# Performance work log

Hardware: AMD Instinct MI355X
Metric: run time of the kernel (lower is better)

The kernel has to match this reference:

```python
import jax, jax.numpy as jnp
import numpy as np
from jax import lax

K = 3
PAD = 1
STRIDE = 1


def setup_inputs() -> dict:
    key = jax.random.key(0)
    k1, k2, k3 = jax.random.split(key, 3)
    B, Cin, Cout, H, W = 4, 64, 64, 128, 128
    x = jax.random.normal(k1, (B, Cin, H, W), dtype=jnp.float32)
    # offset-generating conv weight: [2*K*K, Cin, K, K]
    w_offset = jax.random.normal(k2, (2 * K * K, Cin, K, K), dtype=jnp.float32) * 0.05
    # deformable conv weight: [Cout, Cin, K, K]
    w_deform = jax.random.normal(k3, (Cout, Cin, K, K), dtype=jnp.float32) * 0.05
    return {"x": x, "w_offset": w_offset, "w_deform": w_deform}


def _bilinear_sample_one(img, ys, xs):
    # img: [C, H, W]; ys, xs: [K2, Ho, Wo] float sampling coords
    H, W = img.shape[1], img.shape[2]
    y0 = jnp.floor(ys)
    x0 = jnp.floor(xs)
    wy = ys - y0  # frac weights, [K2, Ho, Wo]
    wx = xs - x0

    def gather(yi, xi):
        valid = (yi >= 0) & (yi <= H - 1) & (xi >= 0) & (xi <= W - 1)
        yc = jnp.clip(yi, 0, H - 1).astype(jnp.int32)
        xc = jnp.clip(xi, 0, W - 1).astype(jnp.int32)
        # img[:, yc, xc] -> [C, K2, Ho, Wo]; zero outside (torchvision zero-pad)
        return img[:, yc, xc] * valid[None].astype(img.dtype)

    v00 = gather(y0, x0)
    v01 = gather(y0, x0 + 1)
    v10 = gather(y0 + 1, x0)
    v11 = gather(y0 + 1, x0 + 1)
    w00 = ((1 - wy) * (1 - wx))[None]
    w01 = ((1 - wy) * wx)[None]
    w10 = (wy * (1 - wx))[None]
    w11 = (wy * wx)[None]
    return v00 * w00 + v01 * w01 + v10 * w10 + v11 * w11  # [C, K2, Ho, Wo]


def reference(x, w_offset, w_deform):
    B, Cin, H, W = x.shape
    Cout = w_deform.shape[0]
    K2 = K * K
    # 1) plain conv to produce offsets: [B, 2*K2, H, W]
    offset = lax.conv_general_dilated(
        x, w_offset, window_strides=(STRIDE, STRIDE),
        padding=((PAD, PAD), (PAD, PAD)),
        dimension_numbers=("NCHW", "OIHW", "NCHW"))
    Ho, Wo = offset.shape[2], offset.shape[3]
    # torchvision ordering: channel 2*k = dy, 2*k+1 = dx, taps row-major
    off = offset.reshape(B, K2, 2, Ho, Wo)
    dy, dx = off[:, :, 0], off[:, :, 1]  # [B, K2, Ho, Wo]
    # 2) base sampling grid per kernel tap
    kk = jnp.arange(K2)
    ki = (kk // K).astype(jnp.float32)  # tap row
    kj = (kk % K).astype(jnp.float32)   # tap col
    base_y = (jnp.arange(Ho, dtype=jnp.float32) * STRIDE - PAD)[None, :] + ki[:, None]  # [K2, Ho]
    base_x = (jnp.arange(Wo, dtype=jnp.float32) * STRIDE - PAD)[None, :] + kj[:, None]  # [K2, Wo]
    ys = base_y[None, :, :, None] + dy  # [B, K2, Ho, Wo]
    xs = base_x[None, :, None, :] + dx
    # 3) deformable bilinear gather: [B, Cin, K2, Ho, Wo]
    sampled = jax.vmap(_bilinear_sample_one)(x, ys, xs)
    # 4) weighted accumulation (the conv contraction)
    out = jnp.einsum("ock,bckhw->bohw", w_deform.reshape(Cout, Cin, K2), sampled)
    return out
```

## Files before the change

kernel.cpp:

```cpp
#include <hip/hip_runtime.h>


#define BATCH 4
#define CIN   64
#define COUT  64
#define HH    128
#define WW    128
#define HWPIX (HH*WW)

typedef __attribute__((ext_vector_type(8))) short short8;
typedef __attribute__((ext_vector_type(4))) float floatx4;

__device__ __forceinline__ unsigned short f2bf(float f) {
  unsigned int u = __float_as_uint(f);
  unsigned int r = u + 0x7fffu + ((u >> 16) & 1u);
  return (unsigned short)(r >> 16);
}
__device__ __forceinline__ float bf2f(unsigned short h) { return __uint_as_float(((unsigned int)h) << 16); }
__device__ __forceinline__ float lo16f(unsigned int u) { return __uint_as_float(u << 16); }
__device__ __forceinline__ float hi16f(unsigned int u) { return __uint_as_float(u & 0xffff0000u); }

__device__ __forceinline__ unsigned int bilin2(unsigned int u00, unsigned int u01,
                                               unsigned int u10, unsigned int u11,
                                               float w00, float w01, float w10, float w11) {
  float lo = w00 * lo16f(u00) + w01 * lo16f(u01) + w10 * lo16f(u10) + w11 * lo16f(u11);
  float hi = w00 * hi16f(u00) + w01 * hi16f(u01) + w10 * hi16f(u10) + w11 * hi16f(u11);
  return (unsigned int)f2bf(lo) | ((unsigned int)f2bf(hi) << 16);
}

__device__ __forceinline__ int swz(int a) { return a ^ (((a >> 9) & 3) << 4); }

__global__ __launch_bounds__(256) void pre_kernel(const float* __restrict__ x,
                                                  const float* __restrict__ wo,
                                                  const float* __restrict__ wd,
                                                  unsigned short* __restrict__ xThi,
                                                  unsigned short* __restrict__ xTlo,
                                                  unsigned short* __restrict__ wdA,
                                                  unsigned short* __restrict__ woAhi,
                                                  unsigned short* __restrict__ woAlo) {
  int tid = threadIdx.x;
  if (blockIdx.x < 4096) {
    __shared__ float tile[32][33];
    int t = blockIdx.x;
    int b = t >> 10, rem = t & 1023;
    int c0 = (rem >> 9) * 32, p0 = (rem & 511) * 32;
    int tx = tid & 31, ty = tid >> 5;
    const float* xb = x + (size_t)b * CIN * HWPIX;
    size_t boff = (size_t)b * HWPIX * CIN;
#pragma unroll
    for (int i = 0; i < 4; i++)
      tile[ty + i * 8][tx] = xb[(size_t)(c0 + ty + i * 8) * HWPIX + p0 + tx];
    __syncthreads();
#pragma unroll
    for (int i = 0; i < 2; i++) {
      int tt = tid + i * 256;
      int row = tt >> 4;
      int cp = tt & 15;
      float v0 = tile[cp * 2][row], v1 = tile[cp * 2 + 1][row];
      unsigned short h0 = f2bf(v0), h1 = f2bf(v1);
      unsigned short l0 = f2bf(v0 - bf2f(h0)), l1 = f2bf(v1 - bf2f(h1));
      size_t o = boff + (size_t)(p0 + row) * CIN + c0 + cp * 2;
      *(ushort2*)&xThi[o] = make_ushort2(h0, h1);
      *(ushort2*)&xTlo[o] = make_ushort2(l0, l1);
    }
  } else {
    int t = (blockIdx.x - 4096) * 256 + tid;
    if (t < 36864) {
      int j = t & 7, lane = (t >> 3) & 63, ct = (t >> 9) & 3, kc = (t >> 11) & 1, kk = t >> 12;
      int cout = ct * 16 + (lane & 15);
      int cin  = kc * 32 + (lane >> 4) * 8 + j;
      wdA[t] = f2bf(wd[(size_t)(cout * CIN + cin) * 9 + kk]);
    }
    int t2 = t - 36864;
    if (t2 >= 0 && t2 < 18432) {
      int j = t2 & 7, lane = (t2 >> 3) & 63, ct = (t2 >> 9) & 1, kc = (t2 >> 10) & 1, kk = t2 >> 11;
      int cout = ct * 16 + (lane & 15);
      int cin  = kc * 32 + (lane >> 4) * 8 + j;
      float v = (cout < 18) ? wo[(size_t)(cout * CIN + cin) * 9 + kk] : 0.f;
      unsigned short h = f2bf(v);
      woAhi[t2] = h;
      woAlo[t2] = f2bf(v - bf2f(h));
    }
  }
}

__global__ __launch_bounds__(256) void fused_dcn_kernel(const unsigned short* __restrict__ xThi,
                                                        const unsigned short* __restrict__ xTlo,
                                                        const unsigned short* __restrict__ woAhi,
                                                        const unsigned short* __restrict__ woAlo,
                                                        const unsigned short* __restrict__ wdA,
                                                        float* __restrict__ out) {
  __shared__ unsigned short sBhi[4096];
  __shared__ unsigned short sBlo[4096];
  __shared__ float offL[18 * 64];

  int tid = threadIdx.x;
  int hw = blockIdx.x;
  int bid = (hw & 7) * 128 + (hw >> 3);
  int b = bid >> 8, r = bid & 255, y = r >> 1, x0 = (r & 1) << 6;

  int p1 = tid >> 2, si = tid & 3;
  int lane = tid & 63, w = tid >> 6;

  const unsigned short* xhib = xThi + (size_t)b * HWPIX * CIN;
  const unsigned short* xlob = xTlo + (size_t)b * HWPIX * CIN;

  int wq = p1 >> 4, iq = p1 & 15;
  int kcd = si >> 1, qb = si & 1;
  int wb0 = ((((wq * 2 + kcd) * 64) + qb * 32 + iq) * 8) * 2;
  int wb1 = wb0 + 256;
  unsigned short* stHi0 = (unsigned short*)((char*)sBhi + swz(wb0));
  unsigned short* stHi1 = (unsigned short*)((char*)sBhi + swz(wb1));
  unsigned short* stLo0 = (unsigned short*)((char*)sBlo + swz(wb0));
  unsigned short* stLo1 = (unsigned short*)((char*)sBlo + swz(wb1));
  int rb0 = (w * 2 + 0) * 1024 + lane * 16;
  int rb1 = (w * 2 + 1) * 1024 + lane * 16;
  const short8* rdHi0 = (const short8*)((const char*)sBhi + swz(rb0));
  const short8* rdHi1 = (const short8*)((const char*)sBhi + swz(rb1));
  const short8* rdLo0 = (const short8*)((const char*)sBlo + swz(rb0));
  const short8* rdLo1 = (const short8*)((const char*)sBlo + swz(rb1));

  int xp = x0 + p1;

  floatx4 oacc[2];
  oacc[0] = (floatx4){0.f, 0.f, 0.f, 0.f};
  oacc[1] = (floatx4){0.f, 0.f, 0.f, 0.f};

  auto ldA = [&](int kk, uint4& h0, uint4& h1, uint4& l0, uint4& l1) {
    int ys = y - 1 + kk / 3;
    int xs = xp - 1 + kk % 3;
    bool valid = (ys >= 0) && (ys < HH) && (xs >= 0) && (xs < WW);
    h0 = (uint4){0, 0, 0, 0}; h1 = h0; l0 = h0; l1 = h0;
    if (valid) {
      const unsigned short* ph = xhib + (size_t)(ys * WW + xs) * CIN + si * 16;
      const unsigned short* pl = xlob + (size_t)(ys * WW + xs) * CIN + si * 16;
      h0 = *(const uint4*)ph; h1 = *(const uint4*)(ph + 8);
      l0 = *(const uint4*)pl; l1 = *(const uint4*)(pl + 8);
    }
  };
  auto bodyA = [&](int kk, const uint4& h0, const uint4& h1, const uint4& l0, const uint4& l1) {
    const short8* Ah = (const short8*)(woAhi + (size_t)kk * 2048);
    const short8* Al = (const short8*)(woAlo + (size_t)kk * 2048);
    short8 ah0a = Ah[lane],       ah1a = Ah[128 + lane];
    short8 al0a = Al[lane],       al1a = Al[128 + lane];
    short8 ah0b = Ah[64 + lane],  ah1b = Ah[192 + lane];
    short8 al0b = Al[64 + lane],  al1b = Al[192 + lane];
    *(uint4*)stHi0 = h0; *(uint4*)stHi1 = h1;
    *(uint4*)stLo0 = l0; *(uint4*)stLo1 = l1;
    __syncthreads();
    short8 bh0 = *rdHi0, bh1 = *rdHi1;
    short8 bl0 = *rdLo0, bl1 = *rdLo1;
    oacc[0] = __builtin_amdgcn_mfma_f32_16x16x32_bf16(ah0a, bh0, oacc[0], 0, 0, 0);
    oacc[0] = __builtin_amdgcn_mfma_f32_16x16x32_bf16(ah0a, bl0, oacc[0], 0, 0, 0);
    oacc[0] = __builtin_amdgcn_mfma_f32_16x16x32_bf16(al0a, bh0, oacc[0], 0, 0, 0);
    oacc[0] = __builtin_amdgcn_mfma_f32_16x16x32_bf16(ah1a, bh1, oacc[0], 0, 0, 0);
    oacc[0] = __builtin_amdgcn_mfma_f32_16x16x32_bf16(ah1a, bl1, oacc[0], 0, 0, 0);
    oacc[0] = __builtin_amdgcn_mfma_f32_16x16x32_bf16(al1a, bh1, oacc[0], 0, 0, 0);
    oacc[1] = __builtin_amdgcn_mfma_f32_16x16x32_bf16(ah0b, bh0, oacc[1], 0, 0, 0);
    oacc[1] = __builtin_amdgcn_mfma_f32_16x16x32_bf16(ah0b, bl0, oacc[1], 0, 0, 0);
    oacc[1] = __builtin_amdgcn_mfma_f32_16x16x32_bf16(al0b, bh0, oacc[1], 0, 0, 0);
    oacc[1] = __builtin_amdgcn_mfma_f32_16x16x32_bf16(ah1b, bh1, oacc[1], 0, 0, 0);
    oacc[1] = __builtin_amdgcn_mfma_f32_16x16x32_bf16(ah1b, bl1, oacc[1], 0, 0, 0);
    oacc[1] = __builtin_amdgcn_mfma_f32_16x16x32_bf16(al1b, bh1, oacc[1], 0, 0, 0);
    __syncthreads();
  };

  {
    uint4 h0c, h1c, l0c, l1c;
    ldA(0, h0c, h1c, l0c, l1c);
#pragma unroll 1
    for (int kk = 0; kk < 8; kk++) {
      uint4 h0n, h1n, l0n, l1n;
      ldA(kk + 1, h0n, h1n, l0n, l1n);
      bodyA(kk, h0c, h1c, l0c, l1c);
      h0c = h0n; h1c = h1n; l0c = l0n; l1c = l1n;
    }
    bodyA(8, h0c, h1c, l0c, l1c);
  }

  {
    int pxl = w * 16 + (lane & 15);
    int rowb = (lane >> 4) * 4;
#pragma unroll
    for (int ct = 0; ct < 2; ct++)
#pragma unroll
      for (int rr = 0; rr < 4; rr++) {
        int row = ct * 16 + rowb + rr;
        if (row < 18) offL[row * 64 + pxl] = oacc[ct][rr];
      }
  }

  floatx4 acc[4];
#pragma unroll
  for (int ct = 0; ct < 4; ct++) acc[ct] = (floatx4){0.f, 0.f, 0.f, 0.f};

  struct BS {
    float w00, w01, w10, w11;
    uint4 a00, a01, a10, a11, b00, b01, b10, b11;
  };
  auto ldB = [&](int kk) -> BS {
    BS s;
    float dy = offL[(2 * kk) * 64 + p1];
    float dx = offL[(2 * kk + 1) * 64 + p1];
    float ys = (float)(y - 1 + kk / 3) + dy;
    float xs = (float)(xp - 1 + kk % 3) + dx;
    float y0f = floorf(ys), x0f = floorf(xs);
    float wy = ys - y0f, wx = xs - x0f;
    int iy0 = (int)y0f, ix0 = (int)x0f;
    int iy1 = iy0 + 1, ix1 = ix0 + 1;
    s.w00 = (1.f - wy) * (1.f - wx); s.w01 = (1.f - wy) * wx;
    s.w10 = wy * (1.f - wx);         s.w11 = wy * wx;
    bool vy0 = (iy0 >= 0) && (iy0 < HH), vy1 = (iy1 >= 0) && (iy1 < HH);
    bool vx0 = (ix0 >= 0) && (ix0 < WW), vx1 = (ix1 >= 0) && (ix1 < WW);
    if (!(vy0 && vx0)) s.w00 = 0.f;
    if (!(vy0 && vx1)) s.w01 = 0.f;
    if (!(vy1 && vx0)) s.w10 = 0.f;
    if (!(vy1 && vx1)) s.w11 = 0.f;
    int cy0 = min(max(iy0, 0), HH - 1), cy1 = min(max(iy1, 0), HH - 1);
    int cx0 = min(max(ix0, 0), WW - 1), cx1 = min(max(ix1, 0), WW - 1);
    const unsigned short* q00 = xhib + (size_t)(cy0 * WW + cx0) * CIN + si * 16;
    const unsigned short* q01 = xhib + (size_t)(cy0 * WW + cx1) * CIN + si * 16;
    const unsigned short* q10 = xhib + (size_t)(cy1 * WW + cx0) * CIN + si * 16;
    const unsigned short* q11 = xhib + (size_t)(cy1 * WW + cx1) * CIN + si * 16;
    s.a00 = *(const uint4*)q00; s.a01 = *(const uint4*)q01;
    s.a10 = *(const uint4*)q10; s.a11 = *(const uint4*)q11;
    s.b00 = *(const uint4*)(q00 + 8); s.b01 = *(const uint4*)(q01 + 8);
    s.b10 = *(const uint4*)(q10 + 8); s.b11 = *(const uint4*)(q11 + 8);
    return s;
  };
  auto bodyB = [&](int kk, const BS& s) {
    const short8* Ap = (const short8*)(wdA + (size_t)kk * 4096);
    short8 a0q0 = Ap[lane],        a1q0 = Ap[256 + lane];
    short8 a0q1 = Ap[64 + lane],   a1q1 = Ap[320 + lane];
    short8 a0q2 = Ap[128 + lane],  a1q2 = Ap[384 + lane];
    short8 a0q3 = Ap[192 + lane],  a1q3 = Ap[448 + lane];
    uint4 o0, o1;
    o0.x = bilin2(s.a00.x, s.a01.x, s.a10.x, s.a11.x, s.w00, s.w01, s.w10, s.w11);
    o0.y = bilin2(s.a00.y, s.a01.y, s.a10.y, s.a11.y, s.w00, s.w01, s.w10, s.w11);
    o0.z = bilin2(s.a00.z, s.a01.z, s.a10.z, s.a11.z, s.w00, s.w01, s.w10, s.w11);
    o0.w = bilin2(s.a00.w, s.a01.w, s.a10.w, s.a11.w, s.w00, s.w01, s.w10, s.w11);
    o1.x = bilin2(s.b00.x, s.b01.x, s.b10.x, s.b11.x, s.w00, s.w01, s.w10, s.w11);
    o1.y = bilin2(s.b00.y, s.b01.y, s.b10.y, s.b11.y, s.w00, s.w01, s.w10, s.w11);
    o1.z = bilin2(s.b00.z, s.b01.z, s.b10.z, s.b11.z, s.w00, s.w01, s.w10, s.w11);
    o1.w = bilin2(s.b00.w, s.b01.w, s.b10.w, s.b11.w, s.w00, s.w01, s.w10, s.w11);
    *(uint4*)stHi0 = o0;
    *(uint4*)stHi1 = o1;
    __syncthreads();
    short8 bv0 = *rdHi0, bv1 = *rdHi1;
    acc[0] = __builtin_amdgcn_mfma_f32_16x16x32_bf16(a0q0, bv0, acc[0], 0, 0, 0);
    acc[0] = __builtin_amdgcn_mfma_f32_16x16x32_bf16(a1q0, bv1, acc[0], 0, 0, 0);
    acc[1] = __builtin_amdgcn_mfma_f32_16x16x32_bf16(a0q1, bv0, acc[1], 0, 0, 0);
    acc[1] = __builtin_amdgcn_mfma_f32_16x16x32_bf16(a1q1, bv1, acc[1], 0, 0, 0);
    acc[2] = __builtin_amdgcn_mfma_f32_16x16x32_bf16(a0q2, bv0, acc[2], 0, 0, 0);
    acc[2] = __builtin_amdgcn_mfma_f32_16x16x32_bf16(a1q2, bv1, acc[2], 0, 0, 0);
    acc[3] = __builtin_amdgcn_mfma_f32_16x16x32_bf16(a0q3, bv0, acc[3], 0, 0, 0);
    acc[3] = __builtin_amdgcn_mfma_f32_16x16x32_bf16(a1q3, bv1, acc[3], 0, 0, 0);
    __syncthreads();
  };

  {
    BS sc = ldB(0);
#pragma unroll 1
    for (int kk = 0; kk < 8; kk++) {
      BS sn = ldB(kk + 1);
      bodyB(kk, sc);
      sc = sn;
    }
    bodyB(8, sc);
  }

  int px = x0 + w * 16 + (lane & 15);
  int rowb = (lane >> 4) * 4;
  float* outb = out + (size_t)b * COUT * HWPIX + y * WW + px;
#pragma unroll
  for (int ct = 0; ct < 4; ct++)
#pragma unroll
    for (int rr = 0; rr < 4; rr++)
      outb[(size_t)(ct * 16 + rowb + rr) * HWPIX] = acc[ct][rr];
}

extern "C" void kernel_launch(void* const* d_in, const int* in_sizes, int n_in,
                              void* d_out, int out_size, void* d_ws, size_t ws_size,
                              hipStream_t stream) {
  const float* x  = (const float*)d_in[0];
  const float* wo = (const float*)d_in[1];
  const float* wd = (const float*)d_in[2];
  float* out = (float*)d_out;

  char* wsb = (char*)d_ws;
  unsigned short* xThi  = (unsigned short*)wsb;
  unsigned short* xTlo  = (unsigned short*)(wsb + 8388608);
  unsigned short* wdA   = (unsigned short*)(wsb + 16777216);
  unsigned short* woAhi = (unsigned short*)(wsb + 16777216 + 73728);
  unsigned short* woAlo = (unsigned short*)(wsb + 16850944 + 36864);

  pre_kernel<<<dim3(4096 + 216), dim3(256), 0, stream>>>(x, wo, wd, xThi, xTlo, wdA, woAhi, woAlo);
  fused_dcn_kernel<<<dim3(BATCH * HWPIX / 64), dim3(256), 0, stream>>>(xThi, xTlo, woAhi, woAlo, wdA, out);
}
```

Measured before the change: 115.5 us.

## Load MFMA B operands directly from global into registers, drop LDS staging

Each lane now fetches the channel slices it needs for its MFMA B fragment: its own pixel column and channel group offset by 8, with a second slice 32 channels further. This removes the shared-memory round trip and both __syncthreads per tap in the offset conv and the deformable conv loops. The cost is that the bilinear interpolation is now done per MFMA lane mapping, with global loads split into smaller, less contiguous 16-byte chunks per pixel. The channel order within the K dimension is permuted, which stays consistent only if the A-fragment weight layout matches.

```diff
diff --git a/kernel.cpp b/kernel.cpp
--- a/kernel.cpp
+++ b/kernel.cpp
@@ -27,8 +27,6 @@
   float hi = w00 * hi16f(u00) + w01 * hi16f(u01) + w10 * hi16f(u10) + w11 * hi16f(u11);
   return (unsigned int)f2bf(lo) | ((unsigned int)f2bf(hi) << 16);
 }
-
-__device__ __forceinline__ int swz(int a) { return a ^ (((a >> 9) & 3) << 4); }
 
 __global__ __launch_bounds__(256) void pre_kernel(const float* __restrict__ x,
                                                   const float* __restrict__ wo,
@@ -90,8 +88,6 @@
                                                         const unsigned short* __restrict__ woAlo,
                                                         const unsigned short* __restrict__ wdA,
                                                         float* __restrict__ out) {
-  __shared__ unsigned short sBhi[4096];
-  __shared__ unsigned short sBlo[4096];
   __shared__ float offL[18 * 64];
 
   int tid = threadIdx.x;
@@ -99,28 +95,14 @@
   int bid = (hw & 7) * 128 + (hw >> 3);
   int b = bid >> 8, r = bid & 255, y = r >> 1, x0 = (r & 1) << 6;
 
-  int p1 = tid >> 2, si = tid & 3;
   int lane = tid & 63, w = tid >> 6;
+  int col = lane & 15, g = lane >> 4;
+  int wcol = w * 16 + col;
+  int px = x0 + wcol;
+  int coff = g * 8;
 
   const unsigned short* xhib = xThi + (size_t)b * HWPIX * CIN;
   const unsigned short* xlob = xTlo + (size_t)b * HWPIX * CIN;
-
-  int wq = p1 >> 4, iq = p1 & 15;
-  int kcd = si >> 1, qb = si & 1;
-  int wb0 = ((((wq * 2 + kcd) * 64) + qb * 32 + iq) * 8) * 2;
-  int wb1 = wb0 + 256;
-  unsigned short* stHi0 = (unsigned short*)((char*)sBhi + swz(wb0));
-  unsigned short* stHi1 = (unsigned short*)((char*)sBhi + swz(wb1));
-  unsigned short* stLo0 = (unsigned short*)((char*)sBlo + swz(wb0));
-  unsigned short* stLo1 = (unsigned short*)((char*)sBlo + swz(wb1));
-  int rb0 = (w * 2 + 0) * 1024 + lane * 16;
-  int rb1 = (w * 2 + 1) * 1024 + lane * 16;
-  const short8* rdHi0 = (const short8*)((const char*)sBhi + swz(rb0));
-  const short8* rdHi1 = (const short8*)((const char*)sBhi + swz(rb1));
-  const short8* rdLo0 = (const short8*)((const char*)sBlo + swz(rb0));
-  const short8* rdLo1 = (const short8*)((const char*)sBlo + swz(rb1));
-
-  int xp = x0 + p1;
 
   floatx4 oacc[2];
   oacc[0] = (floatx4){0.f, 0.f, 0.f, 0.f};
@@ -128,14 +110,14 @@
 
   auto ldA = [&](int kk, uint4& h0, uint4& h1, uint4& l0, uint4& l1) {
     int ys = y - 1 + kk / 3;
-    int xs = xp - 1 + kk % 3;
+    int xs = px - 1 + kk % 3;
     bool valid = (ys >= 0) && (ys < HH) && (xs >= 0) && (xs < WW);
     h0 = (uint4){0, 0, 0, 0}; h1 = h0; l0 = h0; l1 = h0;
     if (valid) {
-      const unsigned short* ph = xhib + (size_t)(ys * WW + xs) * CIN + si * 16;
-      const unsigned short* pl = xlob + (size_t)(ys * WW + xs) * CIN + si * 16;
-      h0 = *(const uint4*)ph; h1 = *(const uint4*)(ph + 8);
-      l0 = *(const uint4*)pl; l1 = *(const uint4*)(pl + 8);
+      const unsigned short* ph = xhib + (size_t)(ys * WW + xs) * CIN + coff;
+      const unsigned short* pl = xlob + (size_t)(ys * WW + xs) * CIN + coff;
+      h0 = *(const uint4*)ph; h1 = *(const uint4*)(ph + 32);
+      l0 = *(const uint4*)pl; l1 = *(const uint4*)(pl + 32);
     }
   };
   auto bodyA = [&](int kk, const uint4& h0, const uint4& h1, const uint4& l0, const uint4& l1) {
@@ -145,11 +127,8 @@
     short8 al0a = Al[lane],       al1a = Al[128 + lane];
     short8 ah0b = Ah[64 + lane],  ah1b = Ah[192 + lane];
     short8 al0b = Al[64 + lane],  al1b = Al[192 + lane];
-    *(uint4*)stHi0 = h0; *(uint4*)stHi1 = h1;
-    *(uint4*)stLo0 = l0; *(uint4*)stLo1 = l1;
-    __syncthreads();
-    short8 bh0 = *rdHi0, bh1 = *rdHi1;
-    short8 bl0 = *rdLo0, bl1 = *rdLo1;
+    short8 bh0 = *(short8*)&h0, bh1 = *(short8*)&h1;
+    short8 bl0 = *(short8*)&l0, bl1 = *(short8*)&l1;
     oacc[0] = __builtin_amdgcn_mfma_f32_16x16x32_bf16(ah0a, bh0, oacc[0], 0, 0, 0);
     oacc[0] = __builtin_amdgcn_mfma_f32_16x16x32_bf16(ah0a, bl0, oacc[0], 0, 0, 0);
     oacc[0] = __builtin_amdgcn_mfma_f32_16x16x32_bf16(al0a, bh0, oacc[0], 0, 0, 0);
@@ -162,7 +141,6 @@
     oacc[1] = __builtin_amdgcn_mfma_f32_16x16x32_bf16(ah1b, bh1, oacc[1], 0, 0, 0);
     oacc[1] = __builtin_amdgcn_mfma_f32_16x16x32_bf16(ah1b, bl1, oacc[1], 0, 0, 0);
     oacc[1] = __builtin_amdgcn_mfma_f32_16x16x32_bf16(al1b, bh1, oacc[1], 0, 0, 0);
-    __syncthreads();
   };
 
   {
@@ -179,14 +157,13 @@
   }
 
   {
-    int pxl = w * 16 + (lane & 15);
-    int rowb = (lane >> 4) * 4;
+    int rowb = g * 4;
 #pragma unroll
     for (int ct = 0; ct < 2; ct++)
 #pragma unroll
       for (int rr = 0; rr < 4; rr++) {
         int row = ct * 16 + rowb + rr;
-        if (row < 18) offL[row * 64 + pxl] = oacc[ct][rr];
+        if (row < 18) offL[row * 64 + wcol] = oacc[ct][rr];
       }
   }
 
@@ -200,10 +177,10 @@
   };
   auto ldB = [&](int kk) -> BS {
     BS s;
-    float dy = offL[(2 * kk) * 64 + p1];
-    float dx = offL[(2 * kk + 1) * 64 + p1];
+    float dy = offL[(2 * kk) * 64 + wcol];
+    float dx = offL[(2 * kk + 1) * 64 + wcol];
     float ys = (float)(y - 1 + kk / 3) + dy;
-    float xs = (float)(xp - 1 + kk % 3) + dx;
+    float xs = (float)(px - 1 + kk % 3) + dx;
     float y0f = floorf(ys), x0f = floorf(xs);
     float wy = ys - y0f, wx = xs - x0f;
     int iy0 = (int)y0f, ix0 = (int)x0f;
@@ -218,14 +195,14 @@
     if (!(vy1 && vx1)) s.w11 = 0.f;
     int cy0 = min(max(iy0, 0), HH - 1), cy1 = min(max(iy1, 0), HH - 1);
     int cx0 = min(max(ix0, 0), WW - 1), cx1 = min(max(ix1, 0), WW - 1);
-    const unsigned short* q00 = xhib + (size_t)(cy0 * WW + cx0) * CIN + si * 16;
-    const unsigned short* q01 = xhib + (size_t)(cy0 * WW + cx1) * CIN + si * 16;
-    const unsigned short* q10 = xhib + (size_t)(cy1 * WW + cx0) * CIN + si * 16;
-    const unsigned short* q11 = xhib + (size_t)(cy1 * WW + cx1) * CIN + si * 16;
+    const unsigned short* q00 = xhib + (size_t)(cy0 * WW + cx0) * CIN + coff;
+    const unsigned short* q01 = xhib + (size_t)(cy0 * WW + cx1) * CIN + coff;
+    const unsigned short* q10 = xhib + (size_t)(cy1 * WW + cx0) * CIN + coff;
+    const unsigned short* q11 = xhib + (size_t)(cy1 * WW + cx1) * CIN + coff;
     s.a00 = *(const uint4*)q00; s.a01 = *(const uint4*)q01;
     s.a10 = *(const uint4*)q10; s.a11 = *(const uint4*)q11;
-    s.b00 = *(const uint4*)(q00 + 8); s.b01 = *(const uint4*)(q01 + 8);
-    s.b10 = *(const uint4*)(q10 + 8); s.b11 = *(const uint4*)(q11 + 8);
+    s.b00 = *(const uint4*)(q00 + 32); s.b01 = *(const uint4*)(q01 + 32);
+    s.b10 = *(const uint4*)(q10 + 32); s.b11 = *(const uint4*)(q11 + 32);
     return s;
   };
   auto bodyB = [&](int kk, const BS& s) {
@@ -243,10 +220,7 @@
     o1.y = bilin2(s.b00.y, s.b01.y, s.b10.y, s.b11.y, s.w00, s.w01, s.w10, s.w11);
     o1.z = bilin2(s.b00.z, s.b01.z, s.b10.z, s.b11.z, s.w00, s.w01, s.w10, s.w11);
     o1.w = bilin2(s.b00.w, s.b01.w, s.b10.w, s.b11.w, s.w00, s.w01, s.w10, s.w11);
-    *(uint4*)stHi0 = o0;
-    *(uint4*)stHi1 = o1;
-    __syncthreads();
-    short8 bv0 = *rdHi0, bv1 = *rdHi1;
+    short8 bv0 = *(short8*)&o0, bv1 = *(short8*)&o1;
     acc[0] = __builtin_amdgcn_mfma_f32_16x16x32_bf16(a0q0, bv0, acc[0], 0, 0, 0);
     acc[0] = __builtin_amdgcn_mfma_f32_16x16x32_bf16(a1q0, bv1, acc[0], 0, 0, 0);
     acc[1] = __builtin_amdgcn_mfma_f32_16x16x32_bf16(a0q1, bv0, acc[1], 0, 0, 0);
@@ -255,7 +229,6 @@
     acc[2] = __builtin_amdgcn_mfma_f32_16x16x32_bf16(a1q2, bv1, acc[2], 0, 0, 0);
     acc[3] = __builtin_amdgcn_mfma_f32_16x16x32_bf16(a0q3, bv0, acc[3], 0, 0, 0);
     acc[3] = __builtin_amdgcn_mfma_f32_16x16x32_bf16(a1q3, bv1, acc[3], 0, 0, 0);
-    __syncthreads();
   };
 
   {
@@ -269,8 +242,7 @@
     bodyB(8, sc);
   }
 
-  int px = x0 + w * 16 + (lane & 15);
-  int rowb = (lane >> 4) * 4;
+  int rowb = g * 4;
   float* outb = out + (size_t)b * COUT * HWPIX + y * WW + px;
 #pragma unroll
   for (int ct = 0; ct < 4; ct++)
```

New measurement: 140.8 us. 22.0% more time.

## Double-buffer LDS staging to halve barriers and use packed bf16 convert

Applied to the files above, without the earlier changes.

The shared-memory B tiles are double-buffered, so each tap stages the next tap's data into the alternate buffer while MFMAs read the current one. This cuts the two barriers per tap down to one and lets the bilinear blend overlap with the matrix work. Separately, the manual round-to-nearest bf16 packing is replaced with a single v_cvt_pk_bf16_f32 instruction. The cost is double the LDS footprint for the staging buffers, which may lower occupancy.

```diff
diff --git a/kernel.cpp b/kernel.cpp
--- a/kernel.cpp
+++ b/kernel.cpp
@@ -25,7 +25,9 @@
                                                float w00, float w01, float w10, float w11) {
   float lo = w00 * lo16f(u00) + w01 * lo16f(u01) + w10 * lo16f(u10) + w11 * lo16f(u11);
   float hi = w00 * hi16f(u00) + w01 * hi16f(u01) + w10 * hi16f(u10) + w11 * hi16f(u11);
-  return (unsigned int)f2bf(lo) | ((unsigned int)f2bf(hi) << 16);
+  unsigned int r;
+  asm("v_cvt_pk_bf16_f32 %0, %1, %2" : "=v"(r) : "v"(lo), "v"(hi));
+  return r;
 }
 
 __device__ __forceinline__ int swz(int a) { return a ^ (((a >> 9) & 3) << 4); }
@@ -90,9 +92,11 @@
                                                         const unsigned short* __restrict__ woAlo,
                                                         const unsigned short* __restrict__ wdA,
                                                         float* __restrict__ out) {
-  __shared__ unsigned short sBhi[4096];
-  __shared__ unsigned short sBlo[4096];
+  __shared__ unsigned short sBhi2[2][4096];
+  __shared__ unsigned short sBlo2[2][4096];
   __shared__ float offL[18 * 64];
+  char* sHc = (char*)sBhi2;
+  char* sLc = (char*)sBlo2;
 
   int tid = threadIdx.x;
   int hw = blockIdx.x;
@@ -109,16 +113,9 @@
   int kcd = si >> 1, qb = si & 1;
   int wb0 = ((((wq * 2 + kcd) * 64) + qb * 32 + iq) * 8) * 2;
   int wb1 = wb0 + 256;
-  unsigned short* stHi0 = (unsigned short*)((char*)sBhi + swz(wb0));
-  unsigned short* stHi1 = (unsigned short*)((char*)sBhi + swz(wb1));
-  unsigned short* stLo0 = (unsigned short*)((char*)sBlo + swz(wb0));
-  unsigned short* stLo1 = (unsigned short*)((char*)sBlo + swz(wb1));
-  int rb0 = (w * 2 + 0) * 1024 + lane * 16;
-  int rb1 = (w * 2 + 1) * 1024 + lane * 16;
-  const short8* rdHi0 = (const short8*)((const char*)sBhi + swz(rb0));
-  const short8* rdHi1 = (const short8*)((const char*)sBhi + swz(rb1));
-  const short8* rdLo0 = (const short8*)((const char*)sBlo + swz(rb0));
-  const short8* rdLo1 = (const short8*)((const char*)sBlo + swz(rb1));
+  int swb0 = swz(wb0), swb1 = swz(wb1);
+  int srb0 = swz((w * 2 + 0) * 1024 + lane * 16);
+  int srb1 = swz((w * 2 + 1) * 1024 + lane * 16);
 
   int xp = x0 + p1;
 
@@ -138,18 +135,23 @@
       l0 = *(const uint4*)pl; l1 = *(const uint4*)(pl + 8);
     }
   };
-  auto bodyA = [&](int kk, const uint4& h0, const uint4& h1, const uint4& l0, const uint4& l1) {
+  auto stageA = [&](int nxt, const uint4& h0, const uint4& h1, const uint4& l0, const uint4& l1) {
+    *(uint4*)(sHc + nxt * 8192 + swb0) = h0;
+    *(uint4*)(sHc + nxt * 8192 + swb1) = h1;
+    *(uint4*)(sLc + nxt * 8192 + swb0) = l0;
+    *(uint4*)(sLc + nxt * 8192 + swb1) = l1;
+  };
+  auto mfmaA = [&](int kk, int cur) {
     const short8* Ah = (const short8*)(woAhi + (size_t)kk * 2048);
     const short8* Al = (const short8*)(woAlo + (size_t)kk * 2048);
     short8 ah0a = Ah[lane],       ah1a = Ah[128 + lane];
     short8 al0a = Al[lane],       al1a = Al[128 + lane];
     short8 ah0b = Ah[64 + lane],  ah1b = Ah[192 + lane];
     short8 al0b = Al[64 + lane],  al1b = Al[192 + lane];
-    *(uint4*)stHi0 = h0; *(uint4*)stHi1 = h1;
-    *(uint4*)stLo0 = l0; *(uint4*)stLo1 = l1;
-    __syncthreads();
-    short8 bh0 = *rdHi0, bh1 = *rdHi1;
-    short8 bl0 = *rdLo0, bl1 = *rdLo1;
+    short8 bh0 = *(const short8*)(sHc + cur * 8192 + srb0);
+    short8 bh1 = *(const short8*)(sHc + cur * 8192 + srb1);
+    short8 bl0 = *(const short8*)(sLc + cur * 8192 + srb0);
+    short8 bl1 = *(const short8*)(sLc + cur * 8192 + srb1);
     oacc[0] = __builtin_amdgcn_mfma_f32_16x16x32_bf16(ah0a, bh0, oacc[0], 0, 0, 0);
     oacc[0] = __builtin_amdgcn_mfma_f32_16x16x32_bf16(ah0a, bl0, oacc[0], 0, 0, 0);
     oacc[0] = __builtin_amdgcn_mfma_f32_16x16x32_bf16(al0a, bh0, oacc[0], 0, 0, 0);
@@ -162,20 +164,21 @@
     oacc[1] = __builtin_amdgcn_mfma_f32_16x16x32_bf16(ah1b, bh1, oacc[1], 0, 0, 0);
     oacc[1] = __builtin_amdgcn_mfma_f32_16x16x32_bf16(ah1b, bl1, oacc[1], 0, 0, 0);
     oacc[1] = __builtin_amdgcn_mfma_f32_16x16x32_bf16(al1b, bh1, oacc[1], 0, 0, 0);
-    __syncthreads();
   };
 
   {
     uint4 h0c, h1c, l0c, l1c;
     ldA(0, h0c, h1c, l0c, l1c);
+    stageA(0, h0c, h1c, l0c, l1c);
+    __syncthreads();
 #pragma unroll 1
-    for (int kk = 0; kk < 8; kk++) {
+    for (int kk = 0; kk < 9; kk++) {
       uint4 h0n, h1n, l0n, l1n;
-      ldA(kk + 1, h0n, h1n, l0n, l1n);
-      bodyA(kk, h0c, h1c, l0c, l1c);
-      h0c = h0n; h1c = h1n; l0c = l0n; l1c = l1n;
-    }
-    bodyA(8, h0c, h1c, l0c, l1c);
+      if (kk < 8) ldA(kk + 1, h0n, h1n, l0n, l1n);
+      mfmaA(kk, kk & 1);
+      if (kk < 8) stageA((kk + 1) & 1, h0n, h1n, l0n, l1n);
+      __syncthreads();
+    }
   }
 
   {
@@ -228,12 +231,7 @@
     s.b10 = *(const uint4*)(q10 + 8); s.b11 = *(const uint4*)(q11 + 8);
     return s;
   };
-  auto bodyB = [&](int kk, const BS& s) {
-    const short8* Ap = (const short8*)(wdA + (size_t)kk * 4096);
-    short8 a0q0 = Ap[lane],        a1q0 = Ap[256 + lane];
-    short8 a0q1 = Ap[64 + lane],   a1q1 = Ap[320 + lane];
-    short8 a0q2 = Ap[128 + lane],  a1q2 = Ap[384 + lane];
-    short8 a0q3 = Ap[192 + lane],  a1q3 = Ap[448 + lane];
+  auto blendStoreB = [&](int nxt, const BS& s) {
     uint4 o0, o1;
     o0.x = bilin2(s.a00.x, s.a01.x, s.a10.x, s.a11.x, s.w00, s.w01, s.w10, s.w11);
     o0.y = bilin2(s.a00.y, s.a01.y, s.a10.y, s.a11.y, s.w00, s.w01, s.w10, s.w11);
@@ -243,10 +241,17 @@
     o1.y = bilin2(s.b00.y, s.b01.y, s.b10.y, s.b11.y, s.w00, s.w01, s.w10, s.w11);
     o1.z = bilin2(s.b00.z, s.b01.z, s.b10.z, s.b11.z, s.w00, s.w01, s.w10, s.w11);
     o1.w = bilin2(s.b00.w, s.b01.w, s.b10.w, s.b11.w, s.w00, s.w01, s.w10, s.w11);
-    *(uint4*)stHi0 = o0;
-    *(uint4*)stHi1 = o1;
-    __syncthreads();
-    short8 bv0 = *rdHi0, bv1 = *rdHi1;
+    *(uint4*)(sHc + nxt * 8192 + swb0) = o0;
+    *(uint4*)(sHc + nxt * 8192 + swb1) = o1;
+  };
+  auto mfmaB = [&](int kk, int cur) {
+    const short8* Ap = (const short8*)(wdA + (size_t)kk * 4096);
+    short8 a0q0 = Ap[lane],        a1q0 = Ap[256 + lane];
+    short8 a0q1 = Ap[64 + lane],   a1q1 = Ap[320 + lane];
+    short8 a0q2 = Ap[128 + lane],  a1q2 = Ap[384 + lane];
+    short8 a0q3 = Ap[192 + lane],  a1q3 = Ap[448 + lane];
+    short8 bv0 = *(const short8*)(sHc + cur * 8192 + srb0);
+    short8 bv1 = *(const short8*)(sHc + cur * 8192 + srb1);
     acc[0] = __builtin_amdgcn_mfma_f32_16x16x32_bf16(a0q0, bv0, acc[0], 0, 0, 0);
     acc[0] = __builtin_amdgcn_mfma_f32_16x16x32_bf16(a1q0, bv1, acc[0], 0, 0, 0);
     acc[1] = __builtin_amdgcn_mfma_f32_16x16x32_bf16(a0q1, bv0, acc[1], 0, 0, 0);
@@ -255,18 +260,20 @@
     acc[2] = __builtin_amdgcn_mfma_f32_16x16x32_bf16(a1q2, bv1, acc[2], 0, 0, 0);
     acc[3] = __builtin_amdgcn_mfma_f32_16x16x32_bf16(a0q3, bv0, acc[3], 0, 0, 0);
     acc[3] = __builtin_amdgcn_mfma_f32_16x16x32_bf16(a1q3, bv1, acc[3], 0, 0, 0);
+  };
+
+  {
+    BS s0 = ldB(0);
+    blendStoreB(0, s0);
     __syncthreads();
-  };
-
-  {
-    BS sc = ldB(0);
 #pragma unroll 1
-    for (int kk = 0; kk < 8; kk++) {
-      BS sn = ldB(kk + 1);
-      bodyB(kk, sc);
-      sc = sn;
-    }
-    bodyB(8, sc);
+    for (int kk = 0; kk < 9; kk++) {
+      BS sn;
+      if (kk < 8) sn = ldB(kk + 1);
+      mfmaB(kk, kk & 1);
+      if (kk < 8) blendStoreB((kk + 1) & 1, sn);
+      __syncthreads();
+    }
   }
 
   int px = x0 + w * 16 + (lane & 15);
```

Result: no change. 115.9 us (+0.3%).
